# Optimization experiments

Hardware: AMD Instinct MI355X
Metric: run time of the kernel (lower is better)

## Reference

```python
import jax, jax.numpy as jnp
import numpy as np

N, D, H, DPE, WALK, L, E = 2048, 512, 8, 16, 8, 3, 32768
HD = D // H
DFF = 4 * D


def setup_inputs() -> dict:
    key = jax.random.key(0)
    ks = jax.random.split(key, 16)
    s = 0.02
    return {
        "node_features": jax.random.normal(ks[0], (N, D), jnp.float32),
        "edge_index": jax.random.randint(ks[1], (2, E), 0, N, dtype=jnp.int32),
        "pe_proj_W": jax.random.normal(ks[2], (WALK, DPE), jnp.float32) * s,
        "pe_proj_b": jnp.zeros((DPE,), jnp.float32),
        "qkv_W": jax.random.normal(ks[3], (L, D, 3 * D), jnp.float32) * s,
        "qkv_b": jnp.zeros((L, 3 * D), jnp.float32),
        "peb_W": jax.random.normal(ks[4], (L, DPE, H), jnp.float32) * s,
        "peb_b": jnp.zeros((L, H), jnp.float32),
        "out_W": jax.random.normal(ks[5], (L, D, D), jnp.float32) * s,
        "out_b": jnp.zeros((L, D), jnp.float32),
        "ffn_W1": jax.random.normal(ks[6], (L, D, DFF), jnp.float32) * s,
        "ffn_b1": jnp.zeros((L, DFF), jnp.float32),
        "ffn_W2": jax.random.normal(ks[7], (L, DFF, D), jnp.float32) * s,
        "ffn_b2": jnp.zeros((L, D), jnp.float32),
        "ln1_g": jnp.ones((L, D), jnp.float32),
        "ln1_b": jnp.zeros((L, D), jnp.float32),
        "ln2_g": jnp.ones((L, D), jnp.float32),
        "ln2_b": jnp.zeros((L, D), jnp.float32),
    }


def _layer_norm(x, g, b, eps=1e-5):
    mu = x.mean(-1, keepdims=True)
    var = ((x - mu) ** 2).mean(-1, keepdims=True)
    return (x - mu) * jax.lax.rsqrt(var + eps) * g + b


def _rw_pe(edge_index, pe_proj_W, pe_proj_b, dtype):
    src, tgt = edge_index[0], edge_index[1]
    adj = jnp.zeros((N, N), dtype).at[src, tgt].set(1.0).at[tgt, src].set(1.0)
    deg = jnp.maximum(adj.sum(axis=1, keepdims=True), 1.0)
    T = adj / deg  # row-stochastic transition matrix

    def step(Tk, _):
        return Tk @ T, jnp.diagonal(Tk)

    _, diags = jax.lax.scan(step, T, None, length=WALK)  # [WALK, N]
    rw = diags.T  # [N, WALK] k-step return probabilities
    return rw @ pe_proj_W + pe_proj_b  # [N, DPE]


def reference(node_features, edge_index, pe_proj_W, pe_proj_b, qkv_W, qkv_b,
              peb_W, peb_b, out_W, out_b, ffn_W1, ffn_b1, ffn_W2, ffn_b2,
              ln1_g, ln1_b, ln2_g, ln2_b):
    pe = _rw_pe(edge_index, pe_proj_W, pe_proj_b, node_features.dtype)
    scale = HD ** -0.5
    x = node_features
    for l in range(L):
        qkv = (x @ qkv_W[l] + qkv_b[l]).reshape(N, 3, H, HD)
        q = jnp.transpose(qkv[:, 0], (1, 0, 2))  # [H, N, HD]
        k = jnp.transpose(qkv[:, 1], (1, 0, 2))
        v = jnp.transpose(qkv[:, 2], (1, 0, 2))
        pe_p = pe @ peb_W[l] + peb_b[l]  # [N, H]
        # bias[h, i, j] = pe_p[i, h] - pe_p[j, h]
        bias = pe_p.T[:, :, None] - pe_p.T[:, None, :]
        scores = jnp.einsum('hnd,hmd->hnm', q, k) * scale + bias
        attn = jax.nn.softmax(scores, axis=-1)
        o = jnp.einsum('hnm,hmd->hnd', attn, v)
        o = jnp.transpose(o, (1, 0, 2)).reshape(N, D) @ out_W[l] + out_b[l]
        x = _layer_norm(x + o, ln1_g[l], ln1_b[l])
        h = jax.nn.gelu(x @ ffn_W1[l] + ffn_b1[l], approximate=False)
        h = h @ ffn_W2[l] + ffn_b2[l]
        x = _layer_norm(x + h, ln2_g[l], ln2_b[l])
    return x
```

## Files before the change

kernel.cpp:

```cpp
#include <hip/hip_runtime.h>
#include <cstdint>
#include <cstddef>

#define NN 2048
#define DM 512
#define NH 8
#define HD 64
#define NL 3
#define NE 32768

typedef unsigned short u16;
typedef unsigned int u32;
typedef __attribute__((ext_vector_type(8))) short short8;
typedef __attribute__((ext_vector_type(4))) float float4v;

__device__ __forceinline__ float bf2f(u16 s){
  union { unsigned u; float f; } v; v.u = ((unsigned)s) << 16; return v.f;
}
__device__ __forceinline__ u16 f2bf(float f){
  union { float f; unsigned u; } v; v.f = f;
  unsigned r = v.u + 0x7fffu + ((v.u >> 16) & 1u);
  return (u16)(r >> 16);
}
__device__ __forceinline__ u16 f2bf_fast(float f){
  union { float f; unsigned u; } v; v.f = f;
  return (u16)((v.u + 0x8000u) >> 16);
}
__device__ __forceinline__ void gl_lds16(const void* g, void* l){
  __builtin_amdgcn_global_load_lds((const __attribute__((address_space(1))) void*)g,
                                   (__attribute__((address_space(3))) void*)l, 16, 0, 0);
}

__global__ void adj_scatter(const int* __restrict__ ei, float* __restrict__ A){
  int e = blockIdx.x*256 + threadIdx.x;
  if (e < NE){
    int s = ei[e], t = ei[NE + e];
    A[(size_t)s*NN + t] = 1.f;
    A[(size_t)t*NN + s] = 1.f;
  }
}

__global__ __launch_bounds__(256)
void rowsum_dinv(const float* __restrict__ A, float* __restrict__ dinv){
  int row = blockIdx.x, tid = threadIdx.x;
  __shared__ float red[4];
  float s = 0.f;
  for (int j=tid;j<NN;j+=256) s += A[(size_t)row*NN + j];
  #pragma unroll
  for (int off=32;off>0;off>>=1) s += __shfl_down(s, off);
  if ((tid&63)==0) red[tid>>6] = s;
  __syncthreads();
  if (tid==0) dinv[row] = rsqrtf(fmaxf(red[0]+red[1]+red[2]+red[3], 1.f));
}

__global__ __launch_bounds__(256)
void build_s_nz(const float* __restrict__ A, const float* __restrict__ dinv,
                u16* __restrict__ S, u32* __restrict__ nz, int* __restrict__ cnt){
  const int i = blockIdx.x, tid = threadIdx.x;
  __shared__ int lc;
  if (tid==0) lc = 0;
  __syncthreads();
  const float di = dinv[i];
  for (int j=tid; j<NN; j+=256){
    float a = A[(size_t)i*NN + j];
    u16 v = f2bf(a * di * dinv[j]);
    S[(size_t)i*NN + j] = v;
    if (v){
      int s = atomicAdd(&lc, 1);
      if (s < 128) nz[i*128 + s] = ((u32)j << 16) | v;
    }
  }
  __syncthreads();
  if (tid==0) cnt[i] = lc < 128 ? lc : 128;
}

__global__ __launch_bounds__(256)
void spmm_sq(const u32* __restrict__ nz, const int* __restrict__ cnt,
             u16* __restrict__ S2)
{
  const int j = blockIdx.x, tid = threadIdx.x;
  __shared__ float row[2048];
  __shared__ u32 lnz[128];
  __shared__ int lcnt;
  for (int c=tid;c<2048;c+=256) row[c] = 0.f;
  if (tid==0) lcnt = cnt[j];
  if (tid<128) lnz[tid] = nz[j*128 + tid];
  __syncthreads();
  const int n = lcnt;
  const int g = tid >> 3, sub = tid & 7;
  for (int e = g; e < n; e += 32){
    u32 p = lnz[e];
    int k = p >> 16;
    float wv = bf2f((u16)(p & 0xffffu));
    int m = cnt[k];
    for (int f = sub; f < m; f += 8){
      u32 qq = nz[k*128 + f];
      atomicAdd(&row[qq >> 16], wv * bf2f((u16)(qq & 0xffffu)));
    }
  }
  __syncthreads();
  short8 o;
  #pragma unroll
  for (int t=0;t<8;t++) o[t] = (short)f2bf(row[tid*8 + t]);
  *(short8*)&S2[(size_t)j*NN + tid*8] = o;
}

__global__ __launch_bounds__(256)
void spmm(const u16* __restrict__ Bold, const u32* __restrict__ nz,
          const int* __restrict__ cnt, u16* __restrict__ Bnew)
{
  const int j = blockIdx.x, tid = threadIdx.x;
  __shared__ u32 lnz[128];
  __shared__ int lcnt;
  if (tid==0) lcnt = cnt[j];
  if (tid<128) lnz[tid] = nz[j*128 + tid];
  __syncthreads();
  const int n = lcnt;
  float acc[8] = {0,0,0,0,0,0,0,0};
  for (int e=0; e<n; e++){
    u32 p = lnz[e];
    int k = p >> 16;
    float wv = bf2f((u16)(p & 0xffffu));
    short8 rv = *(const short8*)&Bold[(size_t)k*NN + tid*8];
    #pragma unroll
    for (int t=0;t<8;t++) acc[t] = fmaf(bf2f((u16)rv[t]), wv, acc[t]);
  }
  short8 o;
  #pragma unroll
  for (int t=0;t<8;t++) o[t] = (short)f2bf(acc[t]);
  *(short8*)&Bnew[(size_t)j*NN + tid*8] = o;
}

__global__ __launch_bounds__(256)
void diag_pe(const u16* __restrict__ S, const u16* __restrict__ S2,
             const u16* __restrict__ S3, const u16* __restrict__ S4,
             const float* __restrict__ peW, const float* __restrict__ peb,
             const float* __restrict__ pebW, const float* __restrict__ pebb,
             float* __restrict__ pebT)
{
  const int i = blockIdx.x, tid = threadIdx.x;
  float d[7] = {0,0,0,0,0,0,0};
  for (int j=tid;j<NN;j+=256){
    float s1 = bf2f(S [(size_t)i*NN + j]);
    float s2 = bf2f(S2[(size_t)i*NN + j]);
    float s3 = bf2f(S3[(size_t)i*NN + j]);
    float s4 = bf2f(S4[(size_t)i*NN + j]);
    d[0] += s1*s1; d[1] += s1*s2; d[2] += s2*s2; d[3] += s2*s3;
    d[4] += s3*s3; d[5] += s3*s4; d[6] += s4*s4;
  }
  __shared__ float red[28];
  __shared__ float pv[16];
  #pragma unroll
  for (int t=0;t<7;t++){
    float v = d[t];
    #pragma unroll
    for (int off=32;off>0;off>>=1) v += __shfl_down(v, off);
    if ((tid&63)==0) red[t*4 + (tid>>6)] = v;
  }
  __syncthreads();
  if (tid < 16){
    float rr[8];
    rr[0] = bf2f(S[(size_t)i*NN + i]);
    #pragma unroll
    for (int t=0;t<7;t++) rr[t+1] = red[t*4]+red[t*4+1]+red[t*4+2]+red[t*4+3];
    float a = peb[tid];
    #pragma unroll
    for (int k=0;k<8;k++) a += rr[k]*peW[k*16 + tid];
    pv[tid] = a;
  }
  __syncthreads();
  if (tid < 24){
    int l = tid >> 3, h = tid & 7;
    float a = pebb[l*NH + h];
    #pragma unroll
    for (int p=0;p<16;p++) a += pv[p]*pebW[(l*16+p)*NH + h];
    pebT[((size_t)l*NH + h)*NN + i] = a;
  }
}

__global__ void init_x(const float* __restrict__ nf, float* __restrict__ x, u16* __restrict__ xbf){
  size_t i = (size_t)blockIdx.x*256 + threadIdx.x;
  float v = nf[i]; x[i] = v; xbf[i] = f2bf(v);
}

__global__ __launch_bounds__(256)
void transpose_all(const float* __restrict__ qkvW, const float* __restrict__ outW,
                   const float* __restrict__ f1W,  const float* __restrict__ f2W,
                   u16* __restrict__ qkvT, u16* __restrict__ outT,
                   u16* __restrict__ f1T,  u16* __restrict__ f2T)
{
  __shared__ float t[32][33];
  int gid = blockIdx.x;
  int l = gid / 3072, r = gid % 3072;
  const float* W; u16* WT; int K, N, bx, by;
  if (r < 768)      { W=qkvW; WT=qkvT; K=512;  N=1536; bx=r%48;        by=r/48; }
  else if (r < 1024){ int u=r-768;  W=outW; WT=outT; K=512;  N=512;  bx=u%16; by=u/16; }
  else if (r < 2048){ int u=r-1024; W=f1W;  WT=f1T;  K=512;  N=2048; bx=u%64; by=u/64; }
  else              { int u=r-2048; W=f2W;  WT=f2T;  K=2048; N=512;  bx=u%16; by=u/16; }
  W  += (size_t)l*K*N;
  WT += (size_t)l*K*N;
  int n0 = bx*32, k0 = by*32;
  int tx = threadIdx.x & 31, ty = threadIdx.x >> 5;
  #pragma unroll
  for (int i=0;i<32;i+=8) t[ty+i][tx] = W[(size_t)(k0+ty+i)*N + n0+tx];
  __syncthreads();
  #pragma unroll
  for (int i=0;i<32;i+=8) WT[(size_t)(n0+ty+i)*K + k0+tx] = f2bf(t[tx][ty+i]);
}

__global__ __launch_bounds__(256)
void ln_kernel(const float* __restrict__ xin, const float* __restrict__ add, int nsl,
               const float* __restrict__ g, const float* __restrict__ b,
               float* __restrict__ xout, u16* __restrict__ xbf)
{
  const int row = blockIdx.x, tid = threadIdx.x;
  __shared__ float red[8];
  const size_t base = (size_t)row*DM;
  float v0 = xin[base+tid];
  float v1 = xin[base+256+tid];
  for (int s=0;s<nsl;s++){
    v0 += add[(size_t)s*NN*DM + base+tid];
    v1 += add[(size_t)s*NN*DM + base+256+tid];
  }
  float s = v0+v1, sq = v0*v0 + v1*v1;
  #pragma unroll
  for (int off=32; off>0; off>>=1){ s += __shfl_down(s, off); sq += __shfl_down(sq, off); }
  if ((tid&63)==0){ red[tid>>6] = s; red[4+(tid>>6)] = sq; }
  __syncthreads();
  float mean = (red[0]+red[1]+red[2]+red[3]) * (1.f/512.f);
  float var  = (red[4]+red[5]+red[6]+red[7]) * (1.f/512.f) - mean*mean;
  float rstd = rsqrtf(var + 1e-5f);
  float y0 = (v0-mean)*rstd*g[tid]     + b[tid];
  float y1 = (v1-mean)*rstd*g[256+tid] + b[256+tid];
  xout[base+tid] = y0;     xout[base+256+tid] = y1;
  xbf[base+tid]  = f2bf(y0); xbf[base+256+tid] = f2bf(y1);
}

template<int OUTMODE, int GELU, int BIAS>
__device__ __forceinline__ void gemm_body(
    u16* As, u16* Bs,
    const u16* __restrict__ A, const u16* __restrict__ BT,
    const float* __restrict__ bias, void* __restrict__ Cout,
    int M, int N, int K, int ldc, int kper, int bm, int bn, int bz)
{
  const int tid = threadIdx.x, lane = tid & 63, wave = tid >> 6;
  const int q = lane >> 4, lo = lane & 15;
  const int wm = wave >> 1, wn = wave & 1;
  const int k_begin = bz * kper;
  const int srow   = lane >> 3;
  const int gchunk = (lane & 7) ^ srow;
  const int woff   = wave * 1024;

  const u16* Ag = A  + ((size_t)bm*64 + 16*wave + srow) * (size_t)K + k_begin + gchunk*8;
  const u16* Bg = BT + ((size_t)bn*64 + 16*wave + srow) * (size_t)K + k_begin + gchunk*8;
  const size_t r8 = (size_t)8 * K;

  float4v acc[2][2] = {};
  const int kiters = kper >> 6;

  gl_lds16(Ag,      As + woff);
  gl_lds16(Ag + r8, As + woff + 512);
  gl_lds16(Bg,      Bs + woff);
  gl_lds16(Bg + r8, Bs + woff + 512);

  for (int it = 0; it < kiters; ++it){
    const int cur = (it & 1) << 12, nxt = cur ^ 4096;
    __syncthreads();
    if (it + 1 < kiters){
      const int ko = (it+1)*64;
      gl_lds16(Ag + ko,      As + nxt + woff);
      gl_lds16(Ag + ko + r8, As + nxt + woff + 512);
      gl_lds16(Bg + ko,      Bs + nxt + woff);
      gl_lds16(Bg + ko + r8, Bs + nxt + woff + 512);
    }
    const short8* Ar = (const short8*)(As + cur);
    const short8* Br = (const short8*)(Bs + cur);
    #pragma unroll
    for (int kk=0;kk<2;kk++){
      const int cx = (kk*4 + q) ^ (lo & 7);
      short8 af[2], bfr[2];
      #pragma unroll
      for (int mt=0;mt<2;mt++) af[mt]  = Ar[(32*wm + 16*mt + lo)*8 + cx];
      #pragma unroll
      for (int nt=0;nt<2;nt++) bfr[nt] = Br[(32*wn + 16*nt + lo)*8 + cx];
      #pragma unroll
      for (int mt=0;mt<2;mt++)
        #pragma unroll
        for (int nt=0;nt<2;nt++)
          acc[mt][nt] = __builtin_amdgcn_mfma_f32_16x16x32_bf16(af[mt], bfr[nt], acc[mt][nt], 0, 0, 0);
    }
  }

  float* Cf = (float*)Cout;
  u16*   Cb = (u16*)Cout;
  const size_t zoff = (OUTMODE == 2) ? (size_t)bz * M * ldc : 0;
  #pragma unroll
  for (int mt=0;mt<2;mt++){
    const int row = bm*64 + 32*wm + 16*mt + q*4;
    #pragma unroll
    for (int nt=0;nt<2;nt++){
      const int col = bn*64 + 32*wn + 16*nt + lo;
      float bbc = (BIAS==1) ? bias[col] : 0.f;
      #pragma unroll
      for (int r=0;r<4;r++){
        float v = acc[mt][nt][r];
        float bb = (BIAS==2) ? bias[row+r] : bbc;
        if (OUTMODE == 2){
          if (BIAS && bz == 0) v += bb;
          Cf[zoff + (size_t)(row+r)*ldc + col] = v;
        } else {
          v += bb;
          if (GELU) v = 0.5f*v*(1.f + erff(v*0.70710678118654752f));
          if (OUTMODE == 1) Cb[(size_t)(row+r)*ldc + col] = f2bf(v);
          else              Cf[(size_t)(row+r)*ldc + col] = v;
        }
      }
    }
  }
}

template<int OUTMODE, int GELU, int BIAS>
__global__ __launch_bounds__(256)
void gemm64(const u16* __restrict__ A, const u16* __restrict__ BT,
            const float* __restrict__ bias, void* __restrict__ Cout,
            int M, int N, int K, int ldc, int kper)
{
  __shared__ u16 As[2*4096];
  __shared__ u16 Bs[2*4096];
  gemm_body<OUTMODE,GELU,BIAS>(As, Bs, A, BT, bias, Cout, M, N, K, ldc, kper,
                               blockIdx.y, blockIdx.x, blockIdx.z);
}

__global__ __launch_bounds__(256)
void qkvt_fused(const u16* __restrict__ xbf, const u16* __restrict__ qkT,
                const float* __restrict__ qkb, u16* __restrict__ qkB,
                const u16* __restrict__ vwT, const float* __restrict__ vb,
                u16* __restrict__ vT)
{
  __shared__ u16 As[2*4096];
  __shared__ u16 Bs[2*4096];
  int id = blockIdx.x;
  if (id < 512)
    gemm_body<1,0,1>(As, Bs, xbf, qkT, qkb, qkB, 2048, 1024, 512, 1024, 512,
                     id >> 4, id & 15, 0);
  else {
    id -= 512;
    gemm_body<1,0,2>(As, Bs, vwT, xbf, vb, vT, 512, 2048, 512, 2048, 512,
                     id >> 5, id & 31, 0);
  }
}

__global__ __launch_bounds__(256)
void attn_part(const u16* __restrict__ qkB, const u16* __restrict__ vT,
               const float* __restrict__ pebT, u16* __restrict__ Opart,
               float* __restrict__ Lsum)
{
  __shared__ u16 Ks[2][64*72];
  __shared__ u16 Vs[2][64*72];
  __shared__ u16 Ps[128*72];
  __shared__ float CB[2][64];
  const int tid = threadIdx.x, lane = tid&63, wave = tid>>6;
  const int q = lane>>4, lo = lane&15;
  const int qb = blockIdx.x, h = blockIdx.y, ks = blockIdx.z;
  const int i0 = qb*128;
  const int part = (ks*NH + h)*16 + qb;

  short8 qf[2][2];
  #pragma unroll
  for (int mt=0;mt<2;mt++)
    #pragma unroll
    for (int kk=0;kk<2;kk++)
      qf[kk][mt] = *(const short8*)&qkB[(size_t)(i0 + 32*wave + 16*mt + lo)*1024 + h*64 + kk*32 + q*8];

  float l_r[2][4] = {};
  float4v o_acc[2][4] = {};

  const int srow = tid >> 2, soff = (tid & 3) * 16;
  const int j_begin = ks*512, j_end = j_begin + 512;

  {
    float4v k0a = *(const float4v*)&qkB[(size_t)(j_begin+srow)*1024 + 512 + h*64 + soff];
    float4v k0b = *(const float4v*)&qkB[(size_t)(j_begin+srow)*1024 + 512 + h*64 + soff + 8];
    float4v v0a = *(const float4v*)&vT[(size_t)(h*64+srow)*NN + j_begin + soff];
    float4v v0b = *(const float4v*)&vT[(size_t)(h*64+srow)*NN + j_begin + soff + 8];
    *(float4v*)&Ks[0][srow*72 + soff]     = k0a;
    *(float4v*)&Ks[0][srow*72 + soff + 8] = k0b;
    *(float4v*)&Vs[0][srow*72 + soff]     = v0a;
    *(float4v*)&Vs[0][srow*72 + soff + 8] = v0b;
    if (tid < 64) CB[0][tid] = pebT[(size_t)h*NN + j_begin + tid] * 1.4426950408889634f;
  }
  __syncthreads();

  for (int j0 = j_begin; j0 < j_end; j0 += 64){
    const int cur = ((j0 - j_begin) >> 6) & 1, nxt = cur ^ 1;
    const bool has_next = (j0 + 64 < j_end);
    float4v ka, kb, va, vb; float cbr = 0.f;
    if (has_next){
      ka = *(const float4v*)&qkB[(size_t)(j0+64+srow)*1024 + 512 + h*64 + soff];
      kb = *(const float4v*)&qkB[(size_t)(j0+64+srow)*1024 + 512 + h*64 + soff + 8];
      va = *(const float4v*)&vT[(size_t)(h*64+srow)*NN + j0+64 + soff];
      vb = *(const float4v*)&vT[(size_t)(h*64+srow)*NN + j0+64 + soff + 8];
      if (tid < 64) cbr = pebT[(size_t)h*NN + j0+64 + tid] * 1.4426950408889634f;
    }

    float4v sacc[2][4] = {};
    const short8* Kr = (const short8*)Ks[cur];
    #pragma unroll
    for (int kk=0; kk<2; kk++){
      #pragma unroll
      for (int nt=0; nt<4; nt++){
        short8 bfr = Kr[(16*nt + lo)*9 + kk*4 + q];
        #pragma unroll
        for (int mt=0; mt<2; mt++)
          sacc[mt][nt] = __builtin_amdgcn_mfma_f32_16x16x32_bf16(qf[kk][mt], bfr, sacc[mt][nt], 0,0,0);
      }
    }
    #pragma unroll
    for (int mt=0; mt<2; mt++)
      #pragma unroll
      for (int nt=0; nt<4; nt++){
        float cb = CB[cur][16*nt + lo];
        #pragma unroll
        for (int r=0;r<4;r++){
          float p = exp2f(fmaf(sacc[mt][nt][r], 0.180336880f, -cb));
          l_r[mt][r] += p;
          Ps[(32*wave + 16*mt + q*4 + r)*72 + 16*nt + lo] = f2bf_fast(p);
        }
      }
    const short8* Pr = (const short8*)Ps;
    const short8* Vr = (const short8*)Vs[cur];
    #pragma unroll
    for (int kk=0;kk<2;kk++){
      #pragma unroll
      for (int mt=0;mt<2;mt++){
        short8 af = Pr[(32*wave + 16*mt + lo)*9 + kk*4 + q];
        #pragma unroll
        for (int nt=0;nt<4;nt++){
          short8 bfr = Vr[(16*nt + lo)*9 + kk*4 + q];
          o_acc[mt][nt] = __builtin_amdgcn_mfma_f32_16x16x32_bf16(af, bfr, o_acc[mt][nt], 0,0,0);
        }
      }
    }
    if (has_next){
      *(float4v*)&Ks[nxt][srow*72 + soff]     = ka;
      *(float4v*)&Ks[nxt][srow*72 + soff + 8] = kb;
      *(float4v*)&Vs[nxt][srow*72 + soff]     = va;
      *(float4v*)&Vs[nxt][srow*72 + soff + 8] = vb;
      if (tid < 64) CB[nxt][tid] = cbr;
    }
    __syncthreads();
  }

  u16* Op = Opart + (size_t)part*8192;
  #pragma unroll
  for (int mt=0;mt<2;mt++){
    #pragma unroll
    for (int r=0;r<4;r++){
      float s = l_r[mt][r];
      s += __shfl_xor(s, 1);
      s += __shfl_xor(s, 2);
      s += __shfl_xor(s, 4);
      s += __shfl_xor(s, 8);
      if (lo == 0) Lsum[part*128 + 32*wave + 16*mt + q*4 + r] = s;
    }
    #pragma unroll
    for (int nt=0;nt<4;nt++)
      #pragma unroll
      for (int r=0;r<4;r++)
        Op[(32*wave + 16*mt + q*4 + r)*64 + 16*nt + lo] = f2bf_fast(o_acc[mt][nt][r]);
  }
}

__global__ __launch_bounds__(256)
void attn_combine(const u16* __restrict__ Opart, const float* __restrict__ Lsum,
                  u16* __restrict__ obuf)
{
  const int qb = blockIdx.x, h = blockIdx.y, tid = threadIdx.x;
  __shared__ float invL[128];
  if (tid < 128){
    float L = 0.f;
    #pragma unroll
    for (int k=0;k<4;k++) L += Lsum[((k*NH + h)*16 + qb)*128 + tid];
    invL[tid] = 1.f / L;
  }
  __syncthreads();
  const int col = tid & 63, r0 = (tid >> 6) * 32;
  #pragma unroll
  for (int r=0;r<32;r++){
    int row = r0 + r;
    float acc = 0.f;
    #pragma unroll
    for (int k=0;k<4;k++)
      acc += bf2f(Opart[((size_t)((k*NH + h)*16 + qb))*8192 + row*64 + col]);
    obuf[(size_t)(qb*128 + row)*DM + h*64 + col] = f2bf(acc * invL[row]);
  }
}

extern "C" void kernel_launch(void* const* d_in, const int* in_sizes, int n_in,
                              void* d_out, int out_size, void* d_ws, size_t ws_size,
                              hipStream_t stream) {
  const float* nf   = (const float*)d_in[0];
  const int*   ei   = (const int*)d_in[1];
  const float* peW  = (const float*)d_in[2];
  const float* peb  = (const float*)d_in[3];
  const float* qkvW = (const float*)d_in[4];
  const float* qkvb = (const float*)d_in[5];
  const float* pebW = (const float*)d_in[6];
  const float* pebb = (const float*)d_in[7];
  const float* outW = (const float*)d_in[8];
  const float* outb = (const float*)d_in[9];
  const float* f1W  = (const float*)d_in[10];
  const float* f1b  = (const float*)d_in[11];
  const float* f2W  = (const float*)d_in[12];
  const float* f2b  = (const float*)d_in[13];
  const float* ln1g = (const float*)d_in[14];
  const float* ln1b = (const float*)d_in[15];
  const float* ln2g = (const float*)d_in[16];
  const float* ln2b = (const float*)d_in[17];
  (void)in_sizes; (void)n_in; (void)out_size; (void)ws_size;

  char* w = (char*)d_ws;
  constexpr size_t OFF_A     = 0;
  constexpr size_t OFF_S     = OFF_A + 16777216;
  constexpr size_t OFF_S2    = OFF_S + 8388608;
  constexpr size_t OFF_S3    = OFF_S2 + 8388608;
  constexpr size_t OFF_S4    = OFF_S3 + 8388608;
  constexpr size_t OFF_DINV  = OFF_S4 + 8388608;
  constexpr size_t OFF_PEBT  = OFF_DINV + 8192;
  constexpr size_t OFF_QKVT  = OFF_PEBT + 196608;
  constexpr size_t OFF_OUTT  = OFF_QKVT + 4718592;
  constexpr size_t OFF_F1T   = OFF_OUTT + 1572864;
  constexpr size_t OFF_F2T   = OFF_F1T + 6291456;
  constexpr size_t OFF_X     = OFF_F2T + 6291456;
  constexpr size_t OFF_XBF   = OFF_X + 4194304;
  constexpr size_t OFF_QKB   = OFF_XBF + 2097152;
  constexpr size_t OFF_VT    = OFF_QKB + 4194304;
  constexpr size_t OFF_OBUF  = OFF_VT + 2097152;
  constexpr size_t OFF_NZ    = OFF_OBUF + 2097152;
  constexpr size_t OFF_CNT   = OFF_NZ + 1048576;
  constexpr size_t OFF_LS    = OFF_CNT + 8192;
  constexpr size_t OFF_HBUF  = OFF_LS + 262144;

  float* A     = (float*)(w + OFF_A);
  u16*   S     = (u16*)  (w + OFF_S);
  u16*   S2    = (u16*)  (w + OFF_S2);
  u16*   S3    = (u16*)  (w + OFF_S3);
  u16*   S4    = (u16*)  (w + OFF_S4);
  float* dinv  = (float*)(w + OFF_DINV);
  float* pebT  = (float*)(w + OFF_PEBT);
  u16*   qkvT  = (u16*)  (w + OFF_QKVT);
  u16*   outT  = (u16*)  (w + OFF_OUTT);
  u16*   f1T   = (u16*)  (w + OFF_F1T);
  u16*   f2T   = (u16*)  (w + OFF_F2T);
  float* x     = (float*)(w + OFF_X);
  u16*   xbf   = (u16*)  (w + OFF_XBF);
  u16*   qkB   = (u16*)  (w + OFF_QKB);
  u16*   vT    = (u16*)  (w + OFF_VT);
  u16*   obuf  = (u16*)  (w + OFF_OBUF);
  u32*   NZ    = (u32*)  (w + OFF_NZ);
  int*   CNT   = (int*)  (w + OFF_CNT);
  float* Lsum  = (float*)(w + OFF_LS);
  u16*   hbuf  = (u16*)  (w + OFF_HBUF);
  u16*   Opart = (u16*)A;

  hipMemsetAsync(A, 0, 16777216, stream);
  adj_scatter<<<dim3(NE/256), 256, 0, stream>>>(ei, A);
  rowsum_dinv<<<dim3(NN), 256, 0, stream>>>(A, dinv);
  build_s_nz<<<dim3(NN), 256, 0, stream>>>(A, dinv, S, NZ, CNT);
  spmm_sq<<<dim3(NN), 256, 0, stream>>>(NZ, CNT, S2);
  spmm<<<dim3(NN), 256, 0, stream>>>(S2, NZ, CNT, S3);
  spmm<<<dim3(NN), 256, 0, stream>>>(S3, NZ, CNT, S4);
  diag_pe<<<dim3(NN), 256, 0, stream>>>(S, S2, S3, S4, peW, peb, pebW, pebb, pebT);

  transpose_all<<<dim3(9216), 256, 0, stream>>>(qkvW, outW, f1W, f2W, qkvT, outT, f1T, f2T);
  init_x<<<dim3(NN*DM/256), 256, 0, stream>>>(nf, x, xbf);

  for (int l = 0; l < NL; l++){
    qkvt_fused<<<dim3(768), 256, 0, stream>>>(
        xbf, qkvT + (size_t)l*1536*512, qkvb + l*1536, qkB,
        qkvT + (size_t)l*1536*512 + (size_t)1024*512, qkvb + l*1536 + 1024, vT);
    attn_part<<<dim3(16,8,4), 256, 0, stream>>>(qkB, vT, pebT + (size_t)l*NH*NN, Opart, Lsum);
    attn_combine<<<dim3(16,8), 256, 0, stream>>>(Opart, Lsum, obuf);

    gemm64<2,0,1><<<dim3(8,32,2), 256, 0, stream>>>(
        obuf, outT + (size_t)l*512*512, outb + l*512, A, 2048, 512, 512, 512, 256);
    ln_kernel<<<dim3(NN), 256, 0, stream>>>(x, A, 2, ln1g + l*512, ln1b + l*512, x, xbf);

    gemm64<1,1,1><<<dim3(32,32,1), 256, 0, stream>>>(
        xbf, f1T + (size_t)l*2048*512, f1b + l*2048, hbuf, 2048, 2048, 512, 2048, 512);
    gemm64<2,0,1><<<dim3(8,32,4), 256, 0, stream>>>(
        hbuf, f2T + (size_t)l*512*2048, f2b + l*512, A, 2048, 512, 2048, 512, 512);
    float* xout = (l == NL-1) ? (float*)d_out : x;
    ln_kernel<<<dim3(NN), 256, 0, stream>>>(x, A, 4, ln2g + l*512, ln2b + l*512, xout, xbf);
  }
}
```

Baseline: 455.9 us.

## Fuse attention combine into out-projection GEMM and shrink GEMM M-tile to 32

Removes the separate attn_combine kernel. The out-projection GEMM now reads the bf16 partial attention outputs and their row sums directly, normalises them and writes the A tile into LDS, so the obuf round trip and one launch go away. All GEMMs change from 64x64 to 32x64 tiles, doubling block counts for better CU occupancy. The FFN2 split-K drops from 4 to 2 slices. The cost is more B reloads per output and lower MFMA reuse per block, and the fused A path uses synchronous register loads instead of async global-to-LDS copies.

```diff
diff --git a/kernel.cpp b/kernel.cpp
--- a/kernel.cpp
+++ b/kernel.cpp
@@ -236,84 +236,127 @@
   xbf[base+tid]  = f2bf(y0); xbf[base+256+tid] = f2bf(y1);
 }
 
-template<int OUTMODE, int GELU, int BIAS>
-__device__ __forceinline__ void gemm_body(
-    u16* As, u16* Bs,
+template<int OUTMODE, int GELU, int BIAS, int ACOMB>
+__device__ __forceinline__ void gemm32_body(
+    u16* As, u16* Bs, float* invLs,
     const u16* __restrict__ A, const u16* __restrict__ BT,
     const float* __restrict__ bias, void* __restrict__ Cout,
+    const u16* __restrict__ Opart, const float* __restrict__ Lsum,
     int M, int N, int K, int ldc, int kper, int bm, int bn, int bz)
 {
   const int tid = threadIdx.x, lane = tid & 63, wave = tid >> 6;
   const int q = lane >> 4, lo = lane & 15;
   const int wm = wave >> 1, wn = wave & 1;
   const int k_begin = bz * kper;
+  const int kiters = kper >> 6;
   const int srow   = lane >> 3;
   const int gchunk = (lane & 7) ^ srow;
-  const int woff   = wave * 1024;
-
-  const u16* Ag = A  + ((size_t)bm*64 + 16*wave + srow) * (size_t)K + k_begin + gchunk*8;
+
   const u16* Bg = BT + ((size_t)bn*64 + 16*wave + srow) * (size_t)K + k_begin + gchunk*8;
   const size_t r8 = (size_t)8 * K;
-
-  float4v acc[2][2] = {};
-  const int kiters = kper >> 6;
-
-  gl_lds16(Ag,      As + woff);
-  gl_lds16(Ag + r8, As + woff + 512);
-  gl_lds16(Bg,      Bs + woff);
-  gl_lds16(Bg + r8, Bs + woff + 512);
+  const int Bwoff = wave * 1024;
+
+  const u16* Ag = nullptr;
+  const int Awoff = wave * 512;
+  if (!ACOMB)
+    Ag = A + ((size_t)bm*32 + wave*8 + srow) * (size_t)K + k_begin + gchunk*8;
+
+  int c_sr=0, c_gc=0, c_qb=0, c_rr=0;
+  if (ACOMB){
+    c_sr = tid >> 3; c_gc = tid & 7;
+    c_qb = bm >> 2; c_rr = (bm & 3)*32 + c_sr;
+    int hh = tid & 7, rr2 = (bm & 3)*32 + (tid >> 3);
+    float L = 0.f;
+    #pragma unroll
+    for (int ks=0;ks<4;ks++)
+      L += Lsum[(((ks*NH + hh)*16 + c_qb))*128 + rr2];
+    invLs[(tid>>3)*8 + hh] = 1.f / L;
+    __syncthreads();
+  }
+
+  float4v acc[2] = {};
+
+  if (ACOMB){
+    const int h0 = bz * kiters;
+    float a8[8] = {0,0,0,0,0,0,0,0};
+    #pragma unroll
+    for (int ks=0;ks<4;ks++){
+      short8 p = *(const short8*)&Opart[((size_t)((ks*NH + h0)*16 + c_qb))*8192 + c_rr*64 + c_gc*8];
+      #pragma unroll
+      for (int t=0;t<8;t++) a8[t] += bf2f((u16)p[t]);
+    }
+    float il = invLs[c_sr*8 + h0 - bz*kiters*0];
+    il = invLs[c_sr*8 + (h0 & 7)];
+    short8 o;
+    #pragma unroll
+    for (int t=0;t<8;t++) o[t] = (short)f2bf_fast(a8[t]*il);
+    *(short8*)&As[c_sr*64 + ((c_gc ^ (c_sr&7))*8)] = o;
+  } else {
+    gl_lds16(Ag, As + Awoff);
+  }
+  gl_lds16(Bg,      Bs + Bwoff);
+  gl_lds16(Bg + r8, Bs + Bwoff + 512);
 
   for (int it = 0; it < kiters; ++it){
-    const int cur = (it & 1) << 12, nxt = cur ^ 4096;
+    const int curA = (it & 1) << 11, nxtA = curA ^ 2048;
+    const int curB = (it & 1) << 12, nxtB = curB ^ 4096;
     __syncthreads();
     if (it + 1 < kiters){
       const int ko = (it+1)*64;
-      gl_lds16(Ag + ko,      As + nxt + woff);
-      gl_lds16(Ag + ko + r8, As + nxt + woff + 512);
-      gl_lds16(Bg + ko,      Bs + nxt + woff);
-      gl_lds16(Bg + ko + r8, Bs + nxt + woff + 512);
-    }
-    const short8* Ar = (const short8*)(As + cur);
-    const short8* Br = (const short8*)(Bs + cur);
+      if (ACOMB){
+        const int h = bz*kiters + it + 1;
+        float a8[8] = {0,0,0,0,0,0,0,0};
+        #pragma unroll
+        for (int ks=0;ks<4;ks++){
+          short8 p = *(const short8*)&Opart[((size_t)((ks*NH + h)*16 + c_qb))*8192 + c_rr*64 + c_gc*8];
+          #pragma unroll
+          for (int t=0;t<8;t++) a8[t] += bf2f((u16)p[t]);
+        }
+        float il = invLs[c_sr*8 + (h & 7)];
+        short8 o;
+        #pragma unroll
+        for (int t=0;t<8;t++) o[t] = (short)f2bf_fast(a8[t]*il);
+        *(short8*)&As[nxtA + c_sr*64 + ((c_gc ^ (c_sr&7))*8)] = o;
+      } else {
+        gl_lds16(Ag + ko, As + nxtA + Awoff);
+      }
+      gl_lds16(Bg + ko,      Bs + nxtB + Bwoff);
+      gl_lds16(Bg + ko + r8, Bs + nxtB + Bwoff + 512);
+    }
+    const short8* Ar = (const short8*)(As + curA);
+    const short8* Br = (const short8*)(Bs + curB);
     #pragma unroll
     for (int kk=0;kk<2;kk++){
       const int cx = (kk*4 + q) ^ (lo & 7);
-      short8 af[2], bfr[2];
+      short8 af = Ar[(16*wm + lo)*8 + cx];
       #pragma unroll
-      for (int mt=0;mt<2;mt++) af[mt]  = Ar[(32*wm + 16*mt + lo)*8 + cx];
-      #pragma unroll
-      for (int nt=0;nt<2;nt++) bfr[nt] = Br[(32*wn + 16*nt + lo)*8 + cx];
-      #pragma unroll
-      for (int mt=0;mt<2;mt++)
-        #pragma unroll
-        for (int nt=0;nt<2;nt++)
-          acc[mt][nt] = __builtin_amdgcn_mfma_f32_16x16x32_bf16(af[mt], bfr[nt], acc[mt][nt], 0, 0, 0);
+      for (int nt=0;nt<2;nt++){
+        short8 bfr = Br[(32*wn + 16*nt + lo)*8 + cx];
+        acc[nt] = __builtin_amdgcn_mfma_f32_16x16x32_bf16(af, bfr, acc[nt], 0, 0, 0);
+      }
     }
   }
 
   float* Cf = (float*)Cout;
   u16*   Cb = (u16*)Cout;
   const size_t zoff = (OUTMODE == 2) ? (size_t)bz * M * ldc : 0;
-  #pragma unroll
-  for (int mt=0;mt<2;mt++){
-    const int row = bm*64 + 32*wm + 16*mt + q*4;
-    #pragma unroll
-    for (int nt=0;nt<2;nt++){
-      const int col = bn*64 + 32*wn + 16*nt + lo;
-      float bbc = (BIAS==1) ? bias[col] : 0.f;
-      #pragma unroll
-      for (int r=0;r<4;r++){
-        float v = acc[mt][nt][r];
-        float bb = (BIAS==2) ? bias[row+r] : bbc;
-        if (OUTMODE == 2){
-          if (BIAS && bz == 0) v += bb;
-          Cf[zoff + (size_t)(row+r)*ldc + col] = v;
-        } else {
-          v += bb;
-          if (GELU) v = 0.5f*v*(1.f + erff(v*0.70710678118654752f));
-          if (OUTMODE == 1) Cb[(size_t)(row+r)*ldc + col] = f2bf(v);
-          else              Cf[(size_t)(row+r)*ldc + col] = v;
-        }
+  const int row = bm*32 + 16*wm + q*4;
+  #pragma unroll
+  for (int nt=0;nt<2;nt++){
+    const int col = bn*64 + 32*wn + 16*nt + lo;
+    float bbc = (BIAS==1) ? bias[col] : 0.f;
+    #pragma unroll
+    for (int r=0;r<4;r++){
+      float v = acc[nt][r];
+      float bb = (BIAS==2) ? bias[row+r] : bbc;
+      if (OUTMODE == 2){
+        if (BIAS && bz == 0) v += bb;
+        Cf[zoff + (size_t)(row+r)*ldc + col] = v;
+      } else {
+        v += bb;
+        if (GELU) v = 0.5f*v*(1.f + erff(v*0.70710678118654752f));
+        if (OUTMODE == 1) Cb[(size_t)(row+r)*ldc + col] = f2bf(v);
+        else              Cf[(size_t)(row+r)*ldc + col] = v;
       }
     }
   }
@@ -321,14 +364,15 @@
 
 template<int OUTMODE, int GELU, int BIAS>
 __global__ __launch_bounds__(256)
-void gemm64(const u16* __restrict__ A, const u16* __restrict__ BT,
+void gemm32(const u16* __restrict__ A, const u16* __restrict__ BT,
             const float* __restrict__ bias, void* __restrict__ Cout,
             int M, int N, int K, int ldc, int kper)
 {
-  __shared__ u16 As[2*4096];
+  __shared__ u16 As[2*2048];
   __shared__ u16 Bs[2*4096];
-  gemm_body<OUTMODE,GELU,BIAS>(As, Bs, A, BT, bias, Cout, M, N, K, ldc, kper,
-                               blockIdx.y, blockIdx.x, blockIdx.z);
+  __shared__ float invLs[256];
+  gemm32_body<OUTMODE,GELU,BIAS,0>(As, Bs, invLs, A, BT, bias, Cout, nullptr, nullptr,
+                                   M, N, K, ldc, kper, blockIdx.y, blockIdx.x, blockIdx.z);
 }
 
 __global__ __launch_bounds__(256)
@@ -337,17 +381,30 @@
                 const u16* __restrict__ vwT, const float* __restrict__ vb,
                 u16* __restrict__ vT)
 {
-  __shared__ u16 As[2*4096];
+  __shared__ u16 As[2*2048];
   __shared__ u16 Bs[2*4096];
+  __shared__ float invLs[256];
   int id = blockIdx.x;
-  if (id < 512)
-    gemm_body<1,0,1>(As, Bs, xbf, qkT, qkb, qkB, 2048, 1024, 512, 1024, 512,
-                     id >> 4, id & 15, 0);
+  if (id < 1024)
+    gemm32_body<1,0,1,0>(As, Bs, invLs, xbf, qkT, qkb, qkB, nullptr, nullptr,
+                         2048, 1024, 512, 1024, 512, id >> 4, id & 15, 0);
   else {
-    id -= 512;
-    gemm_body<1,0,2>(As, Bs, vwT, xbf, vb, vT, 512, 2048, 512, 2048, 512,
-                     id >> 5, id & 31, 0);
-  }
+    id -= 1024;
+    gemm32_body<1,0,2,0>(As, Bs, invLs, vwT, xbf, vb, vT, nullptr, nullptr,
+                         512, 2048, 512, 2048, 512, id >> 5, id & 31, 0);
+  }
+}
+
+__global__ __launch_bounds__(256)
+void outproj_comb(const u16* __restrict__ Opart, const float* __restrict__ Lsum,
+                  const u16* __restrict__ outT, const float* __restrict__ outb,
+                  float* __restrict__ Cslices)
+{
+  __shared__ u16 As[2*2048];
+  __shared__ u16 Bs[2*4096];
+  __shared__ float invLs[256];
+  gemm32_body<2,0,1,1>(As, Bs, invLs, nullptr, outT, outb, Cslices, Opart, Lsum,
+                       2048, 512, 512, 512, 256, blockIdx.y, blockIdx.x, blockIdx.z);
 }
 
 __global__ __launch_bounds__(256)
@@ -468,31 +525,6 @@
       #pragma unroll
       for (int r=0;r<4;r++)
         Op[(32*wave + 16*mt + q*4 + r)*64 + 16*nt + lo] = f2bf_fast(o_acc[mt][nt][r]);
-  }
-}
-
-__global__ __launch_bounds__(256)
-void attn_combine(const u16* __restrict__ Opart, const float* __restrict__ Lsum,
-                  u16* __restrict__ obuf)
-{
-  const int qb = blockIdx.x, h = blockIdx.y, tid = threadIdx.x;
-  __shared__ float invL[128];
-  if (tid < 128){
-    float L = 0.f;
-    #pragma unroll
-    for (int k=0;k<4;k++) L += Lsum[((k*NH + h)*16 + qb)*128 + tid];
-    invL[tid] = 1.f / L;
-  }
-  __syncthreads();
-  const int col = tid & 63, r0 = (tid >> 6) * 32;
-  #pragma unroll
-  for (int r=0;r<32;r++){
-    int row = r0 + r;
-    float acc = 0.f;
-    #pragma unroll
-    for (int k=0;k<4;k++)
-      acc += bf2f(Opart[((size_t)((k*NH + h)*16 + qb))*8192 + row*64 + col]);
-    obuf[(size_t)(qb*128 + row)*DM + h*64 + col] = f2bf(acc * invL[row]);
   }
 }
 
@@ -535,8 +567,7 @@
   constexpr size_t OFF_XBF   = OFF_X + 4194304;
   constexpr size_t OFF_QKB   = OFF_XBF + 2097152;
   constexpr size_t OFF_VT    = OFF_QKB + 4194304;
-  constexpr size_t OFF_OBUF  = OFF_VT + 2097152;
-  constexpr size_t OFF_NZ    = OFF_OBUF + 2097152;
+  constexpr size_t OFF_NZ    = OFF_VT + 2097152;
   constexpr size_t OFF_CNT   = OFF_NZ + 1048576;
   constexpr size_t OFF_LS    = OFF_CNT + 8192;
   constexpr size_t OFF_HBUF  = OFF_LS + 262144;
@@ -556,12 +587,13 @@
   u16*   xbf   = (u16*)  (w + OFF_XBF);
   u16*   qkB   = (u16*)  (w + OFF_QKB);
   u16*   vT    = (u16*)  (w + OFF_VT);
-  u16*   obuf  = (u16*)  (w + OFF_OBUF);
   u32*   NZ    = (u32*)  (w + OFF_NZ);
   int*   CNT   = (int*)  (w + OFF_CNT);
   float* Lsum  = (float*)(w + OFF_LS);
   u16*   hbuf  = (u16*)  (w + OFF_HBUF);
-  u16*   Opart = (u16*)A;
+  u16*   Opart   = (u16*)A;
+  float* Oslices = (float*)(w + OFF_A + 8388608);
+  float* Fslices = (float*)A;
 
   hipMemsetAsync(A, 0, 16777216, stream);
   adj_scatter<<<dim3(NE/256), 256, 0, stream>>>(ei, A);
@@ -576,21 +608,20 @@
   init_x<<<dim3(NN*DM/256), 256, 0, stream>>>(nf, x, xbf);
 
   for (int l = 0; l < NL; l++){
-    qkvt_fused<<<dim3(768), 256, 0, stream>>>(
+    qkvt_fused<<<dim3(1536), 256, 0, stream>>>(
         xbf, qkvT + (size_t)l*1536*512, qkvb + l*1536, qkB,
         qkvT + (size_t)l*1536*512 + (size_t)1024*512, qkvb + l*1536 + 1024, vT);
     attn_part<<<dim3(16,8,4), 256, 0, stream>>>(qkB, vT, pebT + (size_t)l*NH*NN, Opart, Lsum);
-    attn_combine<<<dim3(16,8), 256, 0, stream>>>(Opart, Lsum, obuf);
-
-    gemm64<2,0,1><<<dim3(8,32,2), 256, 0, stream>>>(
-        obuf, outT + (size_t)l*512*512, outb + l*512, A, 2048, 512, 512, 512, 256);
-    ln_kernel<<<dim3(NN), 256, 0, stream>>>(x, A, 2, ln1g + l*512, ln1b + l*512, x, xbf);
-
-    gemm64<1,1,1><<<dim3(32,32,1), 256, 0, stream>>>(
+
+    outproj_comb<<<dim3(8,64,2), 256, 0, stream>>>(
+        Opart, Lsum, outT + (size_t)l*512*512, outb + l*512, Oslices);
+    ln_kernel<<<dim3(NN), 256, 0, stream>>>(x, Oslices, 2, ln1g + l*512, ln1b + l*512, x, xbf);
+
+    gemm32<1,1,1><<<dim3(32,64,1), 256, 0, stream>>>(
         xbf, f1T + (size_t)l*2048*512, f1b + l*2048, hbuf, 2048, 2048, 512, 2048, 512);
-    gemm64<2,0,1><<<dim3(8,32,4), 256, 0, stream>>>(
-        hbuf, f2T + (size_t)l*512*2048, f2b + l*512, A, 2048, 512, 2048, 512, 512);
+    gemm32<2,0,1><<<dim3(8,64,2), 256, 0, stream>>>(
+        hbuf, f2T + (size_t)l*512*2048, f2b + l*512, Fslices, 2048, 512, 2048, 512, 1024);
     float* xout = (l == NL-1) ? (float*)d_out : x;
-    ln_kernel<<<dim3(NN), 256, 0, stream>>>(x, A, 4, ln2g + l*512, ln2b + l*512, xout, xbf);
-  }
-}
+    ln_kernel<<<dim3(NN), 256, 0, stream>>>(x, Fslices, 2, ln2g + l*512, ln2b + l*512, xout, xbf);
+  }
+}
```

Result: no change. 456.5 us (+0.1%).
